# Performance work log

Measured on AMD Instinct MI355X. Metric: run time of the kernel, lower is better.

The kernel has to match this reference:

```python
import jax, jax.numpy as jnp
import numpy as np

N_GENES = 2000
D_MODEL = 256
N_LAYERS = 4
D_STATE = 16
D_CONV = 4
EXPAND = 2
D_INNER = EXPAND * D_MODEL  # 512
DT_RANK = (D_MODEL + 15) // 16  # 16


def layer_norm(x, w, b, eps=1e-5):
    mu = jnp.mean(x, axis=-1, keepdims=True)
    var = jnp.mean((x - mu) ** 2, axis=-1, keepdims=True)
    return (x - mu) * jax.lax.rsqrt(var + eps) * w + b


def mamba_mixer(h, in_w, cw, cb, xp_w, dtp_w, dtp_b, A_log, Dvec, out_w):
    # h: [B, L, d_model]
    B, L, _ = h.shape
    xz = jnp.einsum('bld,ed->ble', h, in_w)            # [B,L,2*Di]
    u, z = jnp.split(xz, 2, axis=-1)                    # [B,L,Di] each
    # causal depthwise conv1d (kernel D_CONV)
    up = jnp.pad(u, ((0, 0), (D_CONV - 1, 0), (0, 0)))
    u = sum(up[:, k:k + L, :] * cw[:, k] for k in range(D_CONV)) + cb
    u = jax.nn.silu(u)
    # input-dependent dt, B, C
    xdbc = jnp.einsum('bld,ed->ble', u, xp_w)           # [B,L,dt_rank+2N]
    dt_r = xdbc[..., :DT_RANK]
    Bm = xdbc[..., DT_RANK:DT_RANK + D_STATE]           # [B,L,N]
    Cm = xdbc[..., DT_RANK + D_STATE:]                  # [B,L,N]
    dt = jax.nn.softplus(jnp.einsum('blr,dr->bld', dt_r, dtp_w) + dtp_b)  # [B,L,Di]
    A = -jnp.exp(A_log)                                 # [Di,N]
    dA = jnp.exp(dt[..., None] * A)                     # [B,L,Di,N]
    dBu = dt[..., None] * Bm[:, :, None, :] * u[..., None]

    def step(hst, inp):
        a, bu = inp
        hst = a * hst + bu
        return hst, hst

    h0 = jnp.zeros((B, D_INNER, D_STATE), dA.dtype)
    _, hs = jax.lax.scan(step, h0, (jnp.moveaxis(dA, 1, 0), jnp.moveaxis(dBu, 1, 0)))
    y = jnp.einsum('lbdn,lbn->bld', hs, jnp.moveaxis(Cm, 1, 0)) + u * Dvec
    y = y * jax.nn.silu(z)
    return jnp.einsum('bld,ed->ble', y, out_w)          # [B,L,d_model]


def setup_inputs() -> dict:
    key = jax.random.key(0)
    ks = jax.random.split(key, 16)
    nl = N_LAYERS
    inp = {
        'x': jax.random.normal(ks[0], (2, N_GENES), jnp.float32),
        'bulk_in_w': jax.random.normal(ks[1], (D_MODEL,), jnp.float32),
        'bulk_in_b': jnp.zeros((D_MODEL,), jnp.float32),
        'gene_emb': jax.random.normal(ks[2], (1, N_GENES, D_MODEL), jnp.float32) * 0.02,
        'mod_emb': jax.random.normal(ks[3], (1, 1, D_MODEL), jnp.float32) * 0.02,
        'ln_w': jnp.ones((nl, D_MODEL), jnp.float32),
        'ln_b': jnp.zeros((nl, D_MODEL), jnp.float32),
        'in_proj_w': jax.random.normal(ks[4], (nl, 2 * D_INNER, D_MODEL), jnp.float32) * (D_MODEL ** -0.5),
        'conv_w': jax.random.normal(ks[5], (nl, D_INNER, D_CONV), jnp.float32) * (D_CONV ** -0.5),
        'conv_b': jnp.zeros((nl, D_INNER), jnp.float32),
        'x_proj_w': jax.random.normal(ks[6], (nl, DT_RANK + 2 * D_STATE, D_INNER), jnp.float32) * (D_INNER ** -0.5),
        'dt_proj_w': jax.random.normal(ks[7], (nl, D_INNER, DT_RANK), jnp.float32) * 0.01,
        'dt_proj_b': jnp.full((nl, D_INNER), -4.0, jnp.float32),
        'A_log': jnp.broadcast_to(jnp.log(jnp.arange(1, D_STATE + 1, dtype=jnp.float32)), (nl, D_INNER, D_STATE)).copy(),
        'D': jnp.ones((nl, D_INNER), jnp.float32),
        'out_proj_w': jax.random.normal(ks[8], (nl, D_MODEL, D_INNER), jnp.float32) * (D_INNER ** -0.5),
        'fin_w': jnp.ones((D_MODEL,), jnp.float32),
        'fin_b': jnp.zeros((D_MODEL,), jnp.float32),
        'head_w': jax.random.normal(ks[9], (D_MODEL,), jnp.float32) * (D_MODEL ** -0.5),
        'head_b': jnp.zeros((), jnp.float32),
    }
    return inp


def reference(x, bulk_in_w, bulk_in_b, gene_emb, mod_emb, ln_w, ln_b, in_proj_w,
              conv_w, conv_b, x_proj_w, dt_proj_w, dt_proj_b, A_log, D, out_proj_w,
              fin_w, fin_b, head_w, head_b):
    # token embed (modality='bulk'); Linear(1,d_model) == x[...,None]*w + b
    h = x[..., None] * bulk_in_w + bulk_in_b + gene_emb + mod_emb  # [B,L,d_model]
    for i in range(N_LAYERS):
        h = h + mamba_mixer(layer_norm(h, ln_w[i], ln_b[i]), in_proj_w[i], conv_w[i],
                            conv_b[i], x_proj_w[i], dt_proj_w[i], dt_proj_b[i],
                            A_log[i], D[i], out_proj_w[i])
    h = layer_norm(h, fin_w, fin_b)
    y = jnp.einsum('bld,d->bl', h, head_w) + head_b  # bulk head, squeeze(-1)
    return y
```

## Files before the change

kernel.cpp:

```cpp
#include <hip/hip_runtime.h>
#include <math.h>

#define B_  2
#define L_  2000
#define DM_ 256
#define DI_ 512
#define DS_ 16
#define NL_ 4
#define BL_ (B_*L_)
#define BLP_ 4096
#define NC_ 125
#define CL_ 16
#define NST_ (B_*DI_*DS_)

typedef unsigned short ushort_t;
typedef __attribute__((ext_vector_type(8))) short bf16x8;
typedef __attribute__((ext_vector_type(4))) float f32x4;

__device__ __forceinline__ float siluf(float x) {
    return x / (1.f + __expf(-x));
}

__device__ __forceinline__ ushort_t f2bf(float x) {
    unsigned int u = __float_as_uint(x);
    unsigned int r = (u + 0x7FFFu + ((u >> 16) & 1u)) >> 16;
    return (ushort_t)r;
}

__device__ __forceinline__ float bf2f(ushort_t v) {
    return __uint_as_float(((unsigned int)v) << 16);
}

__global__ __launch_bounds__(256) void embed_f2bf_kernel(
    const float* __restrict__ x, const float* __restrict__ biw,
    const float* __restrict__ bib, const float* __restrict__ ge,
    const float* __restrict__ me, float* __restrict__ h,
    float2* __restrict__ stats,
    const float* __restrict__ s0, const float* __restrict__ s1,
    const float* __restrict__ s2, ushort_t* __restrict__ d0,
    ushort_t* __restrict__ d1, ushort_t* __restrict__ d2,
    int N0, int N1, int N2)
{
    if (blockIdx.x < BL_) {
        __shared__ float sm[8];
        int bl = blockIdx.x, d = threadIdx.x;
        int l = bl % L_;
        float v = x[bl]*biw[d] + bib[d] + ge[(size_t)l*DM_ + d] + me[d];
        h[(size_t)bl*DM_ + d] = v;
        float s = v, q = v*v;
        #pragma unroll
        for (int o = 32; o > 0; o >>= 1) {
            s += __shfl_down(s, o);
            q += __shfl_down(q, o);
        }
        if ((d & 63) == 0) { sm[d >> 6] = s; sm[4 + (d >> 6)] = q; }
        __syncthreads();
        if (d == 0) {
            stats[bl] = make_float2(sm[0]+sm[1]+sm[2]+sm[3], sm[4]+sm[5]+sm[6]+sm[7]);
            stats[BLP_ + bl]   = make_float2(0.f, 0.f);
            stats[2*BLP_ + bl] = make_float2(0.f, 0.f);
            stats[3*BLP_ + bl] = make_float2(0.f, 0.f);
        }
    } else {
        int i = (blockIdx.x - BL_)*256 + threadIdx.x;
        const float* s; ushort_t* d; int j;
        if (i < N0)           { s = s0; d = d0; j = i; }
        else if (i < N0+N1)   { s = s1; d = d1; j = i - N0; }
        else if (i < N0+N1+N2){ s = s2; d = d2; j = i - N0 - N1; }
        else return;
        float4 v = *(const float4*)(s + 4*j);
        ushort_t o[4] = {f2bf(v.x), f2bf(v.y), f2bf(v.z), f2bf(v.w)};
        *(ushort2*)(d + 4*j)     = *(ushort2*)&o[0];
        *(ushort2*)(d + 4*j + 2) = *(ushort2*)&o[2];
    }
}

__global__ __launch_bounds__(256) void gemm_ln_mfma(
    const float* __restrict__ H, const float2* __restrict__ stats,
    const float* __restrict__ lnw, const float* __restrict__ lnb,
    const ushort_t* __restrict__ W, ushort_t* __restrict__ C, int ldc)
{
    __shared__ ushort_t a_s[128*64];
    __shared__ ushort_t b_s[128*64];
    const int r0 = blockIdx.x*128, c0 = blockIdx.y*128;
    const int tid = threadIdx.x;
    const int lane = tid & 63, w = tid >> 6;
    const int wm = (w & 1)*64, wn = (w >> 1)*64;
    const int qd = lane >> 4, l16 = lane & 15;
    f32x4 acc[4][4] = {};
    for (int kc = 0; kc < DM_; kc += 64) {
        #pragma unroll
        for (int q = 0; q < 4; q++) {
            int ch = tid + 256*q;
            int row = ch >> 3, col8 = (ch & 7)*8;
            int grow = r0 + row;
            float2 t0 = stats[grow], t1 = stats[BLP_ + grow];
            float2 t2 = stats[2*BLP_ + grow], t3 = stats[3*BLP_ + grow];
            float sum = t0.x + t1.x + t2.x + t3.x;
            float ssq = t0.y + t1.y + t2.y + t3.y;
            float mu  = sum * (1.f/DM_);
            float inv = rsqrtf(fmaxf(ssq*(1.f/DM_) - mu*mu, 0.f) + 1e-5f);
            const float* hp = H + (size_t)grow*DM_ + kc + col8;
            float4 h0 = *(const float4*)hp, h1 = *(const float4*)(hp + 4);
            const float* wp = lnw + kc + col8;
            const float* bp = lnb + kc + col8;
            float4 w0 = *(const float4*)wp, w1 = *(const float4*)(wp + 4);
            float4 b0 = *(const float4*)bp, b1 = *(const float4*)(bp + 4);
            __align__(16) ushort_t o[8];
            o[0] = f2bf((h0.x - mu)*inv*w0.x + b0.x);
            o[1] = f2bf((h0.y - mu)*inv*w0.y + b0.y);
            o[2] = f2bf((h0.z - mu)*inv*w0.z + b0.z);
            o[3] = f2bf((h0.w - mu)*inv*w0.w + b0.w);
            o[4] = f2bf((h1.x - mu)*inv*w1.x + b1.x);
            o[5] = f2bf((h1.y - mu)*inv*w1.y + b1.y);
            o[6] = f2bf((h1.z - mu)*inv*w1.z + b1.z);
            o[7] = f2bf((h1.w - mu)*inv*w1.w + b1.w);
            *(uint4*)&a_s[row*64 + col8] = *(const uint4*)o;
            *(bf16x8*)&b_s[row*64 + col8] =
                *(const bf16x8*)(W + (size_t)(c0 + row)*DM_ + kc + col8);
        }
        __syncthreads();
        #pragma unroll
        for (int ks = 0; ks < 2; ks++) {
            bf16x8 af[4], bf[4];
            #pragma unroll
            for (int i = 0; i < 4; i++)
                af[i] = *(const bf16x8*)&a_s[(wm + i*16 + l16)*64 + ks*32 + qd*8];
            #pragma unroll
            for (int j = 0; j < 4; j++)
                bf[j] = *(const bf16x8*)&b_s[(wn + j*16 + l16)*64 + ks*32 + qd*8];
            #pragma unroll
            for (int i = 0; i < 4; i++) {
                #pragma unroll
                for (int j = 0; j < 4; j++)
                    acc[i][j] = __builtin_amdgcn_mfma_f32_16x16x32_bf16(
                        af[i], bf[j], acc[i][j], 0, 0, 0);
            }
        }
        __syncthreads();
    }
    #pragma unroll
    for (int i = 0; i < 4; i++) {
        #pragma unroll
        for (int j = 0; j < 4; j++) {
            #pragma unroll
            for (int r = 0; r < 4; r++) {
                int row = r0 + wm + i*16 + qd*4 + r;
                int col = c0 + wn + j*16 + l16;
                C[(size_t)row*ldc + col] = f2bf(acc[i][j][r]);
            }
        }
    }
}

__global__ __launch_bounds__(256) void conv_xproj_kernel(
    const ushort_t* __restrict__ xz, const float* __restrict__ cw,
    const float* __restrict__ cb, const ushort_t* __restrict__ XWb,
    const float* __restrict__ DTW, const float* __restrict__ DTB,
    const float* __restrict__ Alog,
    ushort_t* __restrict__ u_bf, float* __restrict__ bn,
    float* __restrict__ cn, ushort_t* __restrict__ dtn,
    float2* __restrict__ sa)
{
    __shared__ ushort_t xs[19][520];
    __shared__ ushort_t us[16][520];
    __shared__ float ps[4*16*48];
    __shared__ float dtr_s[16][16];
    const int c = blockIdx.x, b = blockIdx.y;
    const int l0 = c * 16;
    const int tid = threadIdx.x;
    const int lane = tid & 63, w = tid >> 6;
    const int qd = lane >> 4, l16 = lane & 15;
    for (int f = tid; f < 19*64; f += 256) {
        int row = f >> 6, c8 = (f & 63)*8;
        int l = l0 - 3 + row;
        uint4 v = {0u, 0u, 0u, 0u};
        if (l >= 0)
            v = *(const uint4*)(xz + (size_t)(b*L_ + l)*1024 + c8);
        *(uint4*)&xs[row][c8] = v;
    }
    __syncthreads();
    #pragma unroll
    for (int q = 0; q < 2; q++) {
        int ch = tid + q*256;
        float4 wv = *(const float4*)(cw + ch*4);
        float bias = cb[ch];
        float x0 = bf2f(xs[0][ch]);
        float x1 = bf2f(xs[1][ch]);
        float x2 = bf2f(xs[2][ch]);
        #pragma unroll
        for (int j = 0; j < 16; j++) {
            float x3 = bf2f(xs[3 + j][ch]);
            float v = fmaf(x0, wv.x, fmaf(x1, wv.y, fmaf(x2, wv.z, fmaf(x3, wv.w, bias))));
            us[j][ch] = f2bf(siluf(v));
            x0 = x1; x1 = x2; x2 = x3;
        }
    }
    __syncthreads();
    for (int f = tid; f < 16*64; f += 256) {
        int row = f >> 6, c8 = (f & 63)*8;
        *(uint4*)(u_bf + (size_t)(b*L_ + l0 + row)*512 + c8) =
            *(const uint4*)&us[row][c8];
    }
    f32x4 acc[3] = {};
    #pragma unroll
    for (int step = 0; step < 4; step++) {
        int k = w*128 + step*32 + qd*8;
        bf16x8 af = *(const bf16x8*)&us[l16][k];
        #pragma unroll
        for (int j = 0; j < 3; j++) {
            bf16x8 bf = *(const bf16x8*)(XWb + (size_t)(j*16 + l16)*512 + k);
            acc[j] = __builtin_amdgcn_mfma_f32_16x16x32_bf16(af, bf, acc[j], 0, 0, 0);
        }
    }
    #pragma unroll
    for (int j = 0; j < 3; j++) {
        #pragma unroll
        for (int r = 0; r < 4; r++)
            ps[(w*16 + qd*4 + r)*48 + j*16 + l16] = acc[j][r];
    }
    __syncthreads();
    #pragma unroll
    for (int e = tid; e < 768; e += 256)
        ps[e] = ps[e] + ps[768 + e] + ps[1536 + e] + ps[2304 + e];
    __syncthreads();
    {
        int row = tid >> 4, n = tid & 15;
        dtr_s[row][n] = ps[row*48 + n];
        size_t base = ((size_t)(b*L_) + l0 + row)*DS_ + n;
        bn[base] = ps[row*48 + 16 + n];
        cn[base] = ps[row*48 + 32 + n];
    }
    __syncthreads();
    #pragma unroll
    for (int q = 0; q < 2; q++) {
        int d = tid + q*256;
        float wreg[16];
        const float4* wp = (const float4*)(DTW + (size_t)d*16);
        #pragma unroll
        for (int k4 = 0; k4 < 4; k4++) {
            float4 v = wp[k4];
            wreg[4*k4+0] = v.x; wreg[4*k4+1] = v.y;
            wreg[4*k4+2] = v.z; wreg[4*k4+3] = v.w;
        }
        float bias = DTB[d];
        float dtv[16];
        #pragma unroll
        for (int r = 0; r < 16; r++) {
            float a = bias;
            #pragma unroll
            for (int k = 0; k < 16; k++) a = fmaf(dtr_s[r][k], wreg[k], a);
            float dt = a > 20.f ? a : log1pf(__expf(a));
            ushort_t dtb16 = f2bf(dt);
            dtn[((size_t)(b*L_) + l0 + r)*DI_ + d] = dtb16;
            dtv[r] = bf2f(dtb16);
        }
        float Ac[DS_], s[DS_], ap[DS_];
        const float* ar = Alog + (size_t)d*DS_;
        #pragma unroll
        for (int n = 0; n < DS_; n++) { Ac[n] = -__expf(ar[n]); s[n] = 0.f; ap[n] = 1.f; }
        #pragma unroll
        for (int l = 0; l < 16; l++) {
            float dt = dtv[l];
            float u  = bf2f(us[l][d]);
            float dtu = dt*u;
            #pragma unroll
            for (int n = 0; n < DS_; n++) {
                float e = __expf(dt*Ac[n]);
                s[n] = fmaf(e, s[n], dtu*ps[l*48 + 16 + n]);
                ap[n] *= e;
            }
        }
        size_t ib = (((size_t)c*B_ + b)*DI_ + d)*DS_;
        float2* sap = sa + ib;
        #pragma unroll
        for (int k = 0; k < 8; k++) {
            float4 t = make_float4(s[2*k], ap[2*k], s[2*k+1], ap[2*k+1]);
            *(float4*)&sap[2*k] = t;
        }
    }
}

__global__ __launch_bounds__(64) void scan_phase2(
    const float2* __restrict__ sa, float* __restrict__ sinc)
{
    const int t = blockIdx.x*64 + threadIdx.x;
    float s = 0.f;
    for (int g = 0; g < 5; g++) {
        float2 v[25];
        #pragma unroll
        for (int i = 0; i < 25; i++)
            v[i] = sa[(size_t)(g*25 + i)*NST_ + t];
        #pragma unroll
        for (int i = 0; i < 25; i++) {
            sinc[(size_t)(g*25 + i)*NST_ + t] = s;
            s = fmaf(v[i].y, s, v[i].x);
        }
    }
}

template<int LAST>
__global__ __launch_bounds__(512) void phase3_fused(
    const ushort_t* __restrict__ dtn, const ushort_t* __restrict__ u_bf,
    const float* __restrict__ bn, const float* __restrict__ cn,
    const float* __restrict__ Alog, const float* __restrict__ Dv,
    const float* __restrict__ sinc, const ushort_t* __restrict__ xz,
    const ushort_t* __restrict__ opw, float* __restrict__ h,
    const float* __restrict__ lnw, const float* __restrict__ lnb,
    const ushort_t* __restrict__ ipw, ushort_t* __restrict__ xz_out,
    const float* __restrict__ hw, const float* __restrict__ hb,
    float* __restrict__ out)
{
    __shared__ float b_sh[CL_*DS_];
    __shared__ float c_sh[CL_*DS_];
    __shared__ ushort_t ys[16][520];
    __shared__ ushort_t a_sh[16][264];
    __shared__ float2 red2[8*16];
    __shared__ float2 muv[16];
    const int c = blockIdx.x, b = blockIdx.y;
    const int l0 = c*CL_;
    const int tid = threadIdx.x;
    const int w = tid >> 6, lane = tid & 63;
    const int qd = lane >> 4, l16 = lane & 15;
    {
        int f = tid & 255;
        size_t src = ((size_t)(b*L_) + l0)*DS_ + f;
        if (tid < 256) b_sh[f] = bn[src];
        else           c_sh[f] = cn[src];
    }
    const int d = tid;
    float Ac[DS_], s[DS_];
    {
        const float* ar = Alog + (size_t)d*DS_;
        #pragma unroll
        for (int n = 0; n < DS_; n++) Ac[n] = -__expf(ar[n]);
        size_t base = (((size_t)c*B_ + b)*DI_ + d)*DS_;
        #pragma unroll
        for (int n4 = 0; n4 < 4; n4++)
            *(float4*)&s[4*n4] = *(const float4*)(sinc + base + 4*n4);
    }
    const float Dd = Dv[d];
    __syncthreads();
    const ushort_t* dtp = dtn  + ((size_t)(b*L_ + l0))*DI_ + d;
    const ushort_t* up  = u_bf + ((size_t)(b*L_ + l0))*DI_ + d;
    const ushort_t* zp  = xz   + ((size_t)(b*L_ + l0))*1024 + 512 + d;
    for (int l = 0; l < CL_; l++) {
        float dt = bf2f(dtp[(size_t)l*DI_]);
        float u  = bf2f(up[(size_t)l*DI_]);
        float z  = bf2f(zp[(size_t)l*1024]);
        float dtu = dt*u;
        float y = u*Dd;
        #pragma unroll
        for (int n = 0; n < DS_; n++) {
            float e = __expf(dt*Ac[n]);
            s[n] = fmaf(e, s[n], dtu*b_sh[l*DS_ + n]);
            y = fmaf(s[n], c_sh[l*DS_ + n], y);
        }
        ys[l][d] = f2bf(y * siluf(z));
    }
    __syncthreads();
    f32x4 acc[2] = {};
    #pragma unroll
    for (int ks = 0; ks < 16; ks++) {
        bf16x8 af = *(const bf16x8*)&ys[l16][ks*32 + qd*8];
        #pragma unroll
        for (int j = 0; j < 2; j++) {
            bf16x8 bfv = *(const bf16x8*)(opw + (size_t)(w*32 + j*16 + l16)*DI_ + ks*32 + qd*8);
            acc[j] = __builtin_amdgcn_mfma_f32_16x16x32_bf16(af, bfv, acc[j], 0, 0, 0);
        }
    }
    float v[2][4];
    #pragma unroll
    for (int r = 0; r < 4; r++) {
        int lrow = qd*4 + r;
        size_t gr = (size_t)(b*L_ + l0 + lrow);
        float sm = 0.f, sq = 0.f;
        #pragma unroll
        for (int j = 0; j < 2; j++) {
            int col = w*32 + j*16 + l16;
            size_t idx = gr*DM_ + col;
            float vv = h[idx] + acc[j][r];
            if (!LAST) h[idx] = vv;
            v[j][r] = vv;
            sm += vv; sq += vv*vv;
        }
        sm += __shfl_xor(sm, 1); sq += __shfl_xor(sq, 1);
        sm += __shfl_xor(sm, 2); sq += __shfl_xor(sq, 2);
        sm += __shfl_xor(sm, 4); sq += __shfl_xor(sq, 4);
        sm += __shfl_xor(sm, 8); sq += __shfl_xor(sq, 8);
        if (l16 == 0) red2[w*16 + lrow] = make_float2(sm, sq);
    }
    __syncthreads();
    if (tid < 16) {
        float sm = 0.f, sq = 0.f;
        #pragma unroll
        for (int ww = 0; ww < 8; ww++) {
            float2 t = red2[ww*16 + tid];
            sm += t.x; sq += t.y;
        }
        float mu  = sm*(1.f/DM_);
        float inv = rsqrtf(fmaxf(sq*(1.f/DM_) - mu*mu, 0.f) + 1e-5f);
        muv[tid] = make_float2(mu, inv);
    }
    __syncthreads();
    if (!LAST) {
        #pragma unroll
        for (int r = 0; r < 4; r++) {
            int lrow = qd*4 + r;
            float2 mi = muv[lrow];
            #pragma unroll
            for (int j = 0; j < 2; j++) {
                int col = w*32 + j*16 + l16;
                a_sh[lrow][col] = f2bf((v[j][r] - mi.x)*mi.y*lnw[col] + lnb[col]);
            }
        }
        __syncthreads();
        f32x4 acc2[8] = {};
        const int n0 = w*128;
        #pragma unroll
        for (int ks = 0; ks < 8; ks++) {
            bf16x8 af = *(const bf16x8*)&a_sh[l16][ks*32 + qd*8];
            #pragma unroll
            for (int j2 = 0; j2 < 8; j2++) {
                bf16x8 bfv = *(const bf16x8*)(ipw + (size_t)(n0 + j2*16 + l16)*DM_ + ks*32 + qd*8);
                acc2[j2] = __builtin_amdgcn_mfma_f32_16x16x32_bf16(af, bfv, acc2[j2], 0, 0, 0);
            }
        }
        #pragma unroll
        for (int j2 = 0; j2 < 8; j2++) {
            #pragma unroll
            for (int r = 0; r < 4; r++) {
                size_t row = (size_t)(b*L_ + l0 + qd*4 + r);
                xz_out[row*1024 + n0 + j2*16 + l16] = f2bf(acc2[j2][r]);
            }
        }
    } else {
        float hd[4];
        #pragma unroll
        for (int r = 0; r < 4; r++) {
            int lrow = qd*4 + r;
            float2 mi = muv[lrow];
            float a = 0.f;
            #pragma unroll
            for (int j = 0; j < 2; j++) {
                int col = w*32 + j*16 + l16;
                float nv = (v[j][r] - mi.x)*mi.y*lnw[col] + lnb[col];
                a = fmaf(nv, hw[col], a);
            }
            hd[r] = a;
        }
        #pragma unroll
        for (int r = 0; r < 4; r++) {
            float x = hd[r];
            x += __shfl_xor(x, 1); x += __shfl_xor(x, 2);
            x += __shfl_xor(x, 4); x += __shfl_xor(x, 8);
            if (l16 == 0) red2[w*16 + qd*4 + r].x = x;
        }
        __syncthreads();
        if (tid < 16) {
            float x = 0.f;
            #pragma unroll
            for (int ww = 0; ww < 8; ww++) x += red2[ww*16 + tid].x;
            out[(size_t)(b*L_) + l0 + tid] = x + hb[0];
        }
    }
}

extern "C" void kernel_launch(void* const* d_in, const int* in_sizes, int n_in,
                              void* d_out, int out_size, void* d_ws, size_t ws_size,
                              hipStream_t stream)
{
    const float* x    = (const float*)d_in[0];
    const float* biw  = (const float*)d_in[1];
    const float* bib  = (const float*)d_in[2];
    const float* ge   = (const float*)d_in[3];
    const float* me   = (const float*)d_in[4];
    const float* lnw  = (const float*)d_in[5];
    const float* lnb  = (const float*)d_in[6];
    const float* ipw  = (const float*)d_in[7];
    const float* cw   = (const float*)d_in[8];
    const float* cb   = (const float*)d_in[9];
    const float* xpw  = (const float*)d_in[10];
    const float* dtw  = (const float*)d_in[11];
    const float* dtb  = (const float*)d_in[12];
    const float* alog = (const float*)d_in[13];
    const float* Dv   = (const float*)d_in[14];
    const float* opw  = (const float*)d_in[15];
    const float* fw   = (const float*)d_in[16];
    const float* fb   = (const float*)d_in[17];
    const float* hw   = (const float*)d_in[18];
    const float* hb   = (const float*)d_in[19];
    float* out = (float*)d_out;

    float* ws  = (float*)d_ws;
    float* h      = ws;
    float2* stats = (float2*)(h + (size_t)BLP_*DM_);
    float* bn     = (float*)(stats + 4*BLP_);
    float* cn     = bn + (size_t)B_*L_*DS_;
    float2* sa    = (float2*)(cn + (size_t)B_*L_*DS_);
    float* sinc   = (float*)(sa + (size_t)NC_*NST_);
    ushort_t* xz_bf = (ushort_t*)(sinc + (size_t)NC_*NST_);
    ushort_t* u_bf  = xz_bf + (size_t)BLP_*1024;
    ushort_t* dtn   = u_bf + (size_t)BLP_*DI_;
    ushort_t* ipwb  = dtn + (size_t)B_*L_*DI_;
    ushort_t* opwb  = ipwb + (size_t)NL_*1024*DM_;
    ushort_t* xpwb  = opwb + (size_t)NL_*DM_*DI_;

    const int N0 = NL_*1024*DM_/4, N1 = NL_*DM_*DI_/4, N2 = NL_*48*512/4;
    const int conv_blocks = (N0+N1+N2 + 255)/256;
    embed_f2bf_kernel<<<BL_ + conv_blocks, 256, 0, stream>>>(
        x, biw, bib, ge, me, h, stats,
        ipw, opw, xpw, ipwb, opwb, xpwb, N0, N1, N2);

    gemm_ln_mfma<<<dim3(BLP_/128, 1024/128), 256, 0, stream>>>(
        h, stats, lnw, lnb, ipwb, xz_bf, 1024);

    for (int i = 0; i < NL_; i++) {
        conv_xproj_kernel<<<dim3(NC_, B_), 256, 0, stream>>>(
            xz_bf, cw + i*DI_*4, cb + i*DI_, xpwb + (size_t)i*48*512,
            dtw + (size_t)i*DI_*16, dtb + i*DI_, alog + (size_t)i*DI_*DS_,
            u_bf, bn, cn, dtn, sa);
        scan_phase2<<<NST_/64, 64, 0, stream>>>(sa, sinc);
        if (i < NL_-1) {
            phase3_fused<0><<<dim3(NC_, B_), 512, 0, stream>>>(
                dtn, u_bf, bn, cn, alog + (size_t)i*DI_*DS_, Dv + i*DI_,
                sinc, xz_bf, opwb + (size_t)i*DM_*DI_, h,
                lnw + (i+1)*DM_, lnb + (i+1)*DM_,
                ipwb + (size_t)(i+1)*1024*DM_, xz_bf,
                nullptr, nullptr, nullptr);
        } else {
            phase3_fused<1><<<dim3(NC_, B_), 512, 0, stream>>>(
                dtn, u_bf, bn, cn, alog + (size_t)i*DI_*DS_, Dv + i*DI_,
                sinc, xz_bf, opwb + (size_t)i*DM_*DI_, h,
                fw, fb,
                nullptr, xz_bf,
                hw, hb, out);
        }
    }
}
```

Before: 414.3 us.

## Fuse embedding, first LayerNorm and first in-proj GEMM into one kernel

New measurement: 435.7 us. 5.2% more time.

```diff
diff --git a/kernel.cpp b/kernel.cpp
--- a/kernel.cpp
+++ b/kernel.cpp
@@ -31,62 +31,76 @@
     return __uint_as_float(((unsigned int)v) << 16);
 }
 
-__global__ __launch_bounds__(256) void embed_f2bf_kernel(
+__global__ __launch_bounds__(256) void k1_embed_gemm(
     const float* __restrict__ x, const float* __restrict__ biw,
     const float* __restrict__ bib, const float* __restrict__ ge,
-    const float* __restrict__ me, float* __restrict__ h,
-    float2* __restrict__ stats,
-    const float* __restrict__ s0, const float* __restrict__ s1,
-    const float* __restrict__ s2, ushort_t* __restrict__ d0,
-    ushort_t* __restrict__ d1, ushort_t* __restrict__ d2,
-    int N0, int N1, int N2)
+    const float* __restrict__ me,
+    const float* __restrict__ lnw, const float* __restrict__ lnb,
+    const float* __restrict__ ipw, const float* __restrict__ opw,
+    const float* __restrict__ xpw,
+    float* __restrict__ h, ushort_t* __restrict__ C,
+    ushort_t* __restrict__ ipwb, ushort_t* __restrict__ opwb,
+    ushort_t* __restrict__ xpwb)
 {
-    if (blockIdx.x < BL_) {
-        __shared__ float sm[8];
-        int bl = blockIdx.x, d = threadIdx.x;
-        int l = bl % L_;
-        float v = x[bl]*biw[d] + bib[d] + ge[(size_t)l*DM_ + d] + me[d];
-        h[(size_t)bl*DM_ + d] = v;
-        float s = v, q = v*v;
-        #pragma unroll
-        for (int o = 32; o > 0; o >>= 1) {
-            s += __shfl_down(s, o);
-            q += __shfl_down(q, o);
-        }
-        if ((d & 63) == 0) { sm[d >> 6] = s; sm[4 + (d >> 6)] = q; }
-        __syncthreads();
-        if (d == 0) {
-            stats[bl] = make_float2(sm[0]+sm[1]+sm[2]+sm[3], sm[4]+sm[5]+sm[6]+sm[7]);
-            stats[BLP_ + bl]   = make_float2(0.f, 0.f);
-            stats[2*BLP_ + bl] = make_float2(0.f, 0.f);
-            stats[3*BLP_ + bl] = make_float2(0.f, 0.f);
-        }
-    } else {
-        int i = (blockIdx.x - BL_)*256 + threadIdx.x;
+    const int blk = blockIdx.x, tid = threadIdx.x;
+    if (blk >= 256) {
+        const int N0p = 3*1024*DM_/4;
+        const int N1  = NL_*DM_*DI_/4;
+        const int N2  = NL_*48*512/4;
+        int i = (blk - 256)*256 + tid;
         const float* s; ushort_t* d; int j;
-        if (i < N0)           { s = s0; d = d0; j = i; }
-        else if (i < N0+N1)   { s = s1; d = d1; j = i - N0; }
-        else if (i < N0+N1+N2){ s = s2; d = d2; j = i - N0 - N1; }
+        if (i < N0p)          { s = ipw + (size_t)1024*DM_; d = ipwb + (size_t)1024*DM_; j = i; }
+        else if (i < N0p+N1)  { s = opw; d = opwb; j = i - N0p; }
+        else if (i < N0p+N1+N2){ s = xpw; d = xpwb; j = i - N0p - N1; }
         else return;
         float4 v = *(const float4*)(s + 4*j);
         ushort_t o[4] = {f2bf(v.x), f2bf(v.y), f2bf(v.z), f2bf(v.w)};
         *(ushort2*)(d + 4*j)     = *(ushort2*)&o[0];
         *(ushort2*)(d + 4*j + 2) = *(ushort2*)&o[2];
-    }
-}
-
-__global__ __launch_bounds__(256) void gemm_ln_mfma(
-    const float* __restrict__ H, const float2* __restrict__ stats,
-    const float* __restrict__ lnw, const float* __restrict__ lnb,
-    const ushort_t* __restrict__ W, ushort_t* __restrict__ C, int ldc)
-{
+        return;
+    }
     __shared__ ushort_t a_s[128*64];
     __shared__ ushort_t b_s[128*64];
-    const int r0 = blockIdx.x*128, c0 = blockIdx.y*128;
-    const int tid = threadIdx.x;
+    __shared__ float2 smu[128];
+    const int r0 = (blk >> 3)*128, c0 = (blk & 7)*128;
     const int lane = tid & 63, w = tid >> 6;
     const int wm = (w & 1)*64, wn = (w >> 1)*64;
     const int qd = lane >> 4, l16 = lane & 15;
+    {
+        const int row = tid >> 1, hf = tid & 1;
+        const int grow = r0 + row;
+        const bool real = grow < BL_;
+        const int l = grow % L_;
+        const float xv = real ? x[grow] : 0.f;
+        float sum = 0.f, ssq = 0.f;
+        const bool wr = real && (c0 == 0);
+        #pragma unroll 4
+        for (int c4 = 0; c4 < 32; c4++) {
+            int col = hf*128 + c4*4;
+            float4 g  = real ? *(const float4*)(ge + (size_t)l*DM_ + col)
+                             : make_float4(0.f,0.f,0.f,0.f);
+            float4 bw = *(const float4*)(biw + col);
+            float4 bb = *(const float4*)(bib + col);
+            float4 mm = *(const float4*)(me  + col);
+            float4 v;
+            v.x = xv*bw.x + bb.x + g.x + mm.x;
+            v.y = xv*bw.y + bb.y + g.y + mm.y;
+            v.z = xv*bw.z + bb.z + g.z + mm.z;
+            v.w = xv*bw.w + bb.w + g.w + mm.w;
+            if (!real) v = make_float4(0.f,0.f,0.f,0.f);
+            if (wr) *(float4*)(h + (size_t)grow*DM_ + col) = v;
+            sum += v.x + v.y + v.z + v.w;
+            ssq += v.x*v.x + v.y*v.y + v.z*v.z + v.w*v.w;
+        }
+        sum += __shfl_xor(sum, 1);
+        ssq += __shfl_xor(ssq, 1);
+        if (hf == 0) {
+            float mu  = sum * (1.f/DM_);
+            float inv = rsqrtf(fmaxf(ssq*(1.f/DM_) - mu*mu, 0.f) + 1e-5f);
+            smu[row] = make_float2(mu, inv);
+        }
+    }
+    __syncthreads();
     f32x4 acc[4][4] = {};
     for (int kc = 0; kc < DM_; kc += 64) {
         #pragma unroll
@@ -94,30 +108,46 @@
             int ch = tid + 256*q;
             int row = ch >> 3, col8 = (ch & 7)*8;
             int grow = r0 + row;
-            float2 t0 = stats[grow], t1 = stats[BLP_ + grow];
-            float2 t2 = stats[2*BLP_ + grow], t3 = stats[3*BLP_ + grow];
-            float sum = t0.x + t1.x + t2.x + t3.x;
-            float ssq = t0.y + t1.y + t2.y + t3.y;
-            float mu  = sum * (1.f/DM_);
-            float inv = rsqrtf(fmaxf(ssq*(1.f/DM_) - mu*mu, 0.f) + 1e-5f);
-            const float* hp = H + (size_t)grow*DM_ + kc + col8;
-            float4 h0 = *(const float4*)hp, h1 = *(const float4*)(hp + 4);
-            const float* wp = lnw + kc + col8;
-            const float* bp = lnb + kc + col8;
-            float4 w0 = *(const float4*)wp, w1 = *(const float4*)(wp + 4);
-            float4 b0 = *(const float4*)bp, b1 = *(const float4*)(bp + 4);
+            bool real = grow < BL_;
+            int l = grow % L_;
+            float xv = real ? x[grow] : 0.f;
+            float2 mi = smu[row];
+            int col = kc + col8;
+            float4 g0 = real ? *(const float4*)(ge + (size_t)l*DM_ + col)
+                             : make_float4(0.f,0.f,0.f,0.f);
+            float4 g1 = real ? *(const float4*)(ge + (size_t)l*DM_ + col + 4)
+                             : make_float4(0.f,0.f,0.f,0.f);
+            float4 bw0 = *(const float4*)(biw + col), bw1 = *(const float4*)(biw + col + 4);
+            float4 bb0 = *(const float4*)(bib + col), bb1 = *(const float4*)(bib + col + 4);
+            float4 mm0 = *(const float4*)(me  + col), mm1 = *(const float4*)(me  + col + 4);
+            float4 w0 = *(const float4*)(lnw + col), w1 = *(const float4*)(lnw + col + 4);
+            float4 b0 = *(const float4*)(lnb + col), b1 = *(const float4*)(lnb + col + 4);
+            float e0, e1, e2, e3, e4, e5, e6, e7;
+            e0 = xv*bw0.x + bb0.x + g0.x + mm0.x;
+            e1 = xv*bw0.y + bb0.y + g0.y + mm0.y;
+            e2 = xv*bw0.z + bb0.z + g0.z + mm0.z;
+            e3 = xv*bw0.w + bb0.w + g0.w + mm0.w;
+            e4 = xv*bw1.x + bb1.x + g1.x + mm1.x;
+            e5 = xv*bw1.y + bb1.y + g1.y + mm1.y;
+            e6 = xv*bw1.z + bb1.z + g1.z + mm1.z;
+            e7 = xv*bw1.w + bb1.w + g1.w + mm1.w;
+            if (!real) { e0=e1=e2=e3=e4=e5=e6=e7=0.f; }
             __align__(16) ushort_t o[8];
-            o[0] = f2bf((h0.x - mu)*inv*w0.x + b0.x);
-            o[1] = f2bf((h0.y - mu)*inv*w0.y + b0.y);
-            o[2] = f2bf((h0.z - mu)*inv*w0.z + b0.z);
-            o[3] = f2bf((h0.w - mu)*inv*w0.w + b0.w);
-            o[4] = f2bf((h1.x - mu)*inv*w1.x + b1.x);
-            o[5] = f2bf((h1.y - mu)*inv*w1.y + b1.y);
-            o[6] = f2bf((h1.z - mu)*inv*w1.z + b1.z);
-            o[7] = f2bf((h1.w - mu)*inv*w1.w + b1.w);
+            o[0] = f2bf((e0 - mi.x)*mi.y*w0.x + b0.x);
+            o[1] = f2bf((e1 - mi.x)*mi.y*w0.y + b0.y);
+            o[2] = f2bf((e2 - mi.x)*mi.y*w0.z + b0.z);
+            o[3] = f2bf((e3 - mi.x)*mi.y*w0.w + b0.w);
+            o[4] = f2bf((e4 - mi.x)*mi.y*w1.x + b1.x);
+            o[5] = f2bf((e5 - mi.x)*mi.y*w1.y + b1.y);
+            o[6] = f2bf((e6 - mi.x)*mi.y*w1.z + b1.z);
+            o[7] = f2bf((e7 - mi.x)*mi.y*w1.w + b1.w);
             *(uint4*)&a_s[row*64 + col8] = *(const uint4*)o;
-            *(bf16x8*)&b_s[row*64 + col8] =
-                *(const bf16x8*)(W + (size_t)(c0 + row)*DM_ + kc + col8);
+            const float* wp = ipw + (size_t)(c0 + row)*DM_ + col;
+            float4 p0 = *(const float4*)wp, p1 = *(const float4*)(wp + 4);
+            __align__(16) ushort_t ob[8];
+            ob[0] = f2bf(p0.x); ob[1] = f2bf(p0.y); ob[2] = f2bf(p0.z); ob[3] = f2bf(p0.w);
+            ob[4] = f2bf(p1.x); ob[5] = f2bf(p1.y); ob[6] = f2bf(p1.z); ob[7] = f2bf(p1.w);
+            *(uint4*)&b_s[row*64 + col8] = *(const uint4*)ob;
         }
         __syncthreads();
         #pragma unroll
@@ -147,7 +177,7 @@
             for (int r = 0; r < 4; r++) {
                 int row = r0 + wm + i*16 + qd*4 + r;
                 int col = c0 + wn + j*16 + l16;
-                C[(size_t)row*ldc + col] = f2bf(acc[i][j][r]);
+                C[(size_t)row*1024 + col] = f2bf(acc[i][j][r]);
             }
         }
     }
@@ -451,17 +481,17 @@
         }
         #pragma unroll
         for (int r = 0; r < 4; r++) {
-            float x = hd[r];
-            x += __shfl_xor(x, 1); x += __shfl_xor(x, 2);
-            x += __shfl_xor(x, 4); x += __shfl_xor(x, 8);
-            if (l16 == 0) red2[w*16 + qd*4 + r].x = x;
+            float xv = hd[r];
+            xv += __shfl_xor(xv, 1); xv += __shfl_xor(xv, 2);
+            xv += __shfl_xor(xv, 4); xv += __shfl_xor(xv, 8);
+            if (l16 == 0) red2[w*16 + qd*4 + r].x = xv;
         }
         __syncthreads();
         if (tid < 16) {
-            float x = 0.f;
-            #pragma unroll
-            for (int ww = 0; ww < 8; ww++) x += red2[ww*16 + tid].x;
-            out[(size_t)(b*L_) + l0 + tid] = x + hb[0];
+            float xv = 0.f;
+            #pragma unroll
+            for (int ww = 0; ww < 8; ww++) xv += red2[ww*16 + tid].x;
+            out[(size_t)(b*L_) + l0 + tid] = xv + hb[0];
         }
     }
 }
@@ -494,8 +524,7 @@
 
     float* ws  = (float*)d_ws;
     float* h      = ws;
-    float2* stats = (float2*)(h + (size_t)BLP_*DM_);
-    float* bn     = (float*)(stats + 4*BLP_);
+    float* bn     = h + (size_t)BLP_*DM_;
     float* cn     = bn + (size_t)B_*L_*DS_;
     float2* sa    = (float2*)(cn + (size_t)B_*L_*DS_);
     float* sinc   = (float*)(sa + (size_t)NC_*NST_);
@@ -506,14 +535,10 @@
     ushort_t* opwb  = ipwb + (size_t)NL_*1024*DM_;
     ushort_t* xpwb  = opwb + (size_t)NL_*DM_*DI_;
 
-    const int N0 = NL_*1024*DM_/4, N1 = NL_*DM_*DI_/4, N2 = NL_*48*512/4;
-    const int conv_blocks = (N0+N1+N2 + 255)/256;
-    embed_f2bf_kernel<<<BL_ + conv_blocks, 256, 0, stream>>>(
-        x, biw, bib, ge, me, h, stats,
-        ipw, opw, xpw, ipwb, opwb, xpwb, N0, N1, N2);
-
-    gemm_ln_mfma<<<dim3(BLP_/128, 1024/128), 256, 0, stream>>>(
-        h, stats, lnw, lnb, ipwb, xz_bf, 1024);
+    const int NCV = (3*1024*DM_/4 + NL_*DM_*DI_/4 + NL_*48*512/4 + 255)/256;
+    k1_embed_gemm<<<256 + NCV, 256, 0, stream>>>(
+        x, biw, bib, ge, me, lnw, lnb, ipw, opw, xpw,
+        h, xz_bf, ipwb, opwb, xpwb);
 
     for (int i = 0; i < NL_; i++) {
         conv_xproj_kernel<<<dim3(NC_, B_), 256, 0, stream>>>(
```
